# Optimization experiments

Measured on AMD Instinct MI355X. Metric: run time of the kernel, lower is better.

The kernel has to match this reference:

```python
import jax, jax.numpy as jnp
import numpy as np

D_MODEL = 1024
D_STATE = 128
D_CONV = 4
EXPAND = 2
HEADDIM = 64
D_INNER = EXPAND * D_MODEL          # 2048
NHEADS = D_INNER // HEADDIM          # 32
CONV_CH = D_INNER + 2 * D_STATE      # conv acts on x, B, C (ngroups=1)
D_IN_PROJ = 2 * D_INNER + 2 * D_STATE + NHEADS
CHUNK = 128


def setup_inputs() -> dict:
    key = jax.random.key(0)
    ks = jax.random.split(key, 8)
    B, L = 4, 2048
    return {
        'x': jax.random.normal(ks[0], (B, L, D_MODEL), jnp.float32),
        'ln_w': jnp.ones((D_MODEL,), jnp.float32),
        'ln_b': jnp.zeros((D_MODEL,), jnp.float32),
        'in_proj_w': jax.random.normal(ks[1], (D_IN_PROJ, D_MODEL), jnp.float32) * 0.02,
        'conv_w': jax.random.normal(ks[2], (CONV_CH, D_CONV), jnp.float32) * 0.2,
        'conv_b': jnp.zeros((CONV_CH,), jnp.float32),
        'dt_bias': jax.random.normal(ks[3], (NHEADS,), jnp.float32) * 0.5,
        'A_log': jax.random.uniform(ks[4], (NHEADS,), jnp.float32, 0.0, 1.5),
        'D': jax.random.normal(ks[5], (NHEADS,), jnp.float32) * 0.1 + 1.0,
        'norm_w': jnp.ones((D_INNER,), jnp.float32),
        'out_proj_w': jax.random.normal(ks[6], (D_MODEL, D_INNER), jnp.float32) * 0.02,
    }


def segsum(a):
    # a: (..., T) -> (..., T, T) with out[i, j] = sum_{j < k <= i} a[k], -inf above diag
    T = a.shape[-1]
    a_rep = jnp.broadcast_to(a[..., :, None], a.shape + (T,))
    a_masked = jnp.where(jnp.tril(jnp.ones((T, T), bool), -1), a_rep, 0.0)
    seg = jnp.cumsum(a_masked, axis=-2)
    return jnp.where(jnp.tril(jnp.ones((T, T), bool), 0), seg, -jnp.inf)


def _ssd(X, a, Bm, Cm):
    # Chunked SSD (Mamba2). X: (b,l,h,p) pre-multiplied by dt; a: (b,l,h)=dt*A; Bm,Cm: (b,l,n)
    b, l, h, p = X.shape
    c = l // CHUNK
    Xc = X.reshape(b, c, CHUNK, h, p)
    Bc = Bm.reshape(b, c, CHUNK, -1)
    Cc = Cm.reshape(b, c, CHUNK, -1)
    ac = a.reshape(b, c, CHUNK, h).transpose(0, 3, 1, 2)   # (b,h,c,q)
    a_cs = jnp.cumsum(ac, axis=-1)                          # (b,h,c,q)
    Lm = jnp.exp(segsum(ac))                                # (b,h,c,q,q)
    # intra-chunk (diagonal) part
    Y_diag = jnp.einsum('bcln,bcsn,bhcls,bcshp->bclhp', Cc, Bc, Lm, Xc)
    # chunk final states
    decay_states = jnp.exp(a_cs[..., -1:] - a_cs)           # (b,h,c,q)
    states = jnp.einsum('bcln,bhcl,bclhp->bchpn', Bc, decay_states, Xc)
    states = jnp.concatenate([jnp.zeros_like(states[:, :1]), states], axis=1)  # (b,c+1,h,p,n)
    a_chunk = jnp.pad(a_cs[..., -1], ((0, 0), (0, 0), (1, 0)))  # (b,h,c+1)
    decay_chunk = jnp.exp(segsum(a_chunk))                  # (b,h,c+1,c+1)
    prev_states = jnp.einsum('bhzc,bchpn->bzhpn', decay_chunk, states)[:, :-1]  # (b,c,h,p,n)
    # inter-chunk (off-diagonal) part
    Y_off = jnp.einsum('bcln,bchpn,bhcl->bclhp', Cc, prev_states, jnp.exp(a_cs))
    return (Y_diag + Y_off).reshape(b, l, h, p)


def reference(x, ln_w, ln_b, in_proj_w, conv_w, conv_b, dt_bias, A_log, D, norm_w, out_proj_w):
    B, L, _ = x.shape
    # pre-LayerNorm
    mu = x.mean(-1, keepdims=True)
    var = ((x - mu) ** 2).mean(-1, keepdims=True)
    h = (x - mu) / jnp.sqrt(var + 1e-5) * ln_w + ln_b
    # Mamba2 in_proj -> [z, xBC, dt]
    zxbcdt = h @ in_proj_w.T
    z = zxbcdt[..., :D_INNER]
    xBC = zxbcdt[..., D_INNER:D_INNER + CONV_CH]
    dt = jax.nn.softplus(zxbcdt[..., -NHEADS:] + dt_bias)  # (B,L,H)
    # causal depthwise conv1d + SiLU
    xp = jnp.pad(xBC, ((0, 0), (D_CONV - 1, 0), (0, 0)))
    conv = sum(xp[:, k:k + L, :] * conv_w[:, k] for k in range(D_CONV)) + conv_b
    xBC = jax.nn.silu(conv)
    xs = xBC[..., :D_INNER].reshape(B, L, NHEADS, HEADDIM)
    Bm = xBC[..., D_INNER:D_INNER + D_STATE]
    Cm = xBC[..., D_INNER + D_STATE:]
    A = -jnp.exp(A_log)                                    # (H,)
    Y = _ssd(xs * dt[..., None], dt * A, Bm, Cm)
    Y = Y + D[None, None, :, None] * xs                    # D skip connection
    y = Y.reshape(B, L, D_INNER)
    # gated RMSNorm (norm_before_gate=False)
    y = y * jax.nn.silu(z)
    y = y * jax.lax.rsqrt(jnp.mean(y * y, -1, keepdims=True) + 1e-5) * norm_w
    out = y @ out_proj_w.T
    # dropout in eval mode = identity; residual
    return out + x
```

## Files before the change

### kernel.cpp

```cpp
#include <hip/hip_runtime.h>
#include <math.h>

#define BATCH   4
#define LSEQ    2048
#define DMODEL  1024
#define DSTATE  128
#define HEADDIM 64
#define DINNER  2048
#define NHEADS  32
#define CONVCH  2304
#define DINPROJ 4384
#define NPAD    4480
#define CHUNKL  128
#define NCHUNK  16
#define ROWS    (BATCH*LSEQ)

#define B_Z     ((size_t)0)
#define B_XBC   (B_Z   + (size_t)ROWS*DINNER*2)
#define B_DT    (B_XBC + (size_t)ROWS*CONVCH*2)
#define B_XS    (B_DT  + (size_t)ROWS*NHEADS*4)
#define B_BC    (B_XS  + (size_t)ROWS*DINNER*2)
#define B_Y     (B_BC  + (size_t)ROWS*256*2)
#define B_ASUM  (B_Y   + (size_t)ROWS*DINNER*2)
#define B_END   (B_ASUM + (size_t)BATCH*NCHUNK*NHEADS*4)

typedef __attribute__((ext_vector_type(8))) short bf16x8;
typedef __attribute__((ext_vector_type(4))) float f32x4;

__device__ __forceinline__ float b2f(ushort u) {
  union { uint32_t i; float f; } v; v.i = ((uint32_t)u) << 16; return v.f;
}
__device__ __forceinline__ ushort f2b(float f) {
  union { float f; uint32_t i; } v; v.f = f;
  uint32_t r = (v.i + 0x7FFFu + ((v.i >> 16) & 1u)) >> 16;
  return (ushort)r;
}

__device__ __forceinline__ void async_ld16(const void* g, void* l) {
  __builtin_amdgcn_global_load_lds(
      (const __attribute__((address_space(1))) unsigned int*)g,
      (__attribute__((address_space(3))) unsigned int*)l, 16, 0, 0);
}

__global__ __launch_bounds__(256) void convert_win_kernel(const float* __restrict__ W,
                                                          ushort* __restrict__ Wb)
{
  size_t i = (size_t)blockIdx.x*256 + threadIdx.x;
  Wb[i] = (i < (size_t)DINPROJ*DMODEL) ? f2b(W[i]) : (ushort)0;
}

__global__ __launch_bounds__(256) void convert_wout_kernel(const float* __restrict__ W,
                                                           ushort* __restrict__ Wb)
{
  size_t i = (size_t)blockIdx.x*256 + threadIdx.x;
  Wb[i] = f2b(W[i]);
}

__global__ __launch_bounds__(256) void ln_kernel(const float* __restrict__ x,
    const float* __restrict__ w, const float* __restrict__ bias, ushort* __restrict__ h)
{
  const int row = blockIdx.x;
  const int t = threadIdx.x;
  const float* xr = x + (size_t)row * DMODEL;
  float v[4];
  float s = 0.f;
  #pragma unroll
  for (int i = 0; i < 4; i++) { v[i] = xr[t + i*256]; s += v[i]; }
  __shared__ float red[4];
  #pragma unroll
  for (int o = 32; o > 0; o >>= 1) s += __shfl_down(s, o, 64);
  if ((t & 63) == 0) red[t >> 6] = s;
  __syncthreads();
  float mean = (red[0]+red[1]+red[2]+red[3]) * (1.f/DMODEL);
  float vs = 0.f;
  #pragma unroll
  for (int i = 0; i < 4; i++) { float d = v[i]-mean; vs += d*d; }
  #pragma unroll
  for (int o = 32; o > 0; o >>= 1) vs += __shfl_down(vs, o, 64);
  __syncthreads();
  if ((t & 63) == 0) red[t >> 6] = vs;
  __syncthreads();
  float rstd = rsqrtf((red[0]+red[1]+red[2]+red[3]) * (1.f/DMODEL) + 1e-5f);
  ushort* hr = h + (size_t)row * DMODEL;
  #pragma unroll
  for (int i = 0; i < 4; i++) {
    int c = t + i*256;
    hr[c] = f2b((v[i]-mean)*rstd*w[c] + bias[c]);
  }
}

__global__ __launch_bounds__(256) void gemm_inproj_mfma(const ushort* __restrict__ A,
    const ushort* __restrict__ W, ushort* __restrict__ z, ushort* __restrict__ xbc,
    float* __restrict__ dtr)
{
  constexpr int K = DMODEL;
  __shared__ ushort smem[128*136];
  ushort* lA = smem;
  ushort* lB = smem + 4096;
  const int tid = threadIdx.x;
  const int lane = tid & 63;
  const int w = tid >> 6;
  const int m0 = blockIdx.x * 128;
  const int n0 = blockIdx.y * 128;
  const int wm = (w & 1) * 64;
  const int wn = (w >> 1) * 64;
  f32x4 acc[4][4];
  #pragma unroll
  for (int i = 0; i < 4; i++)
    #pragma unroll
    for (int j = 0; j < 4; j++) acc[i][j] = (f32x4)(0.f);

  for (int k0 = 0; k0 < K; k0 += 32) {
    __syncthreads();
    #pragma unroll
    for (int is = 0; is < 2; is++) {
      int c = w*128 + is*64 + lane;
      int row = c >> 2, cb = c & 3;
      async_ld16(A + (size_t)(m0 + row)*K + k0 + cb*8, lA + (size_t)(w*128 + is*64)*8);
      async_ld16(W + (size_t)(n0 + row)*K + k0 + cb*8, lB + (size_t)(w*128 + is*64)*8);
    }
    __syncthreads();
    bf16x8 af[4], bfr[4];
    #pragma unroll
    for (int i = 0; i < 4; i++)
      af[i] = *(const bf16x8*)&lA[(wm + i*16 + (lane & 15))*32 + (lane >> 4)*8];
    #pragma unroll
    for (int j = 0; j < 4; j++)
      bfr[j] = *(const bf16x8*)&lB[(wn + j*16 + (lane & 15))*32 + (lane >> 4)*8];
    #pragma unroll
    for (int i = 0; i < 4; i++)
      #pragma unroll
      for (int j = 0; j < 4; j++)
        acc[i][j] = __builtin_amdgcn_mfma_f32_16x16x32_bf16(af[i], bfr[j], acc[i][j], 0, 0, 0);
  }

  const int col_l = lane & 15;
  const int row_l = (lane >> 4) * 4;
  __syncthreads();
  if (n0 < DINNER + CONVCH) {
    #pragma unroll
    for (int i = 0; i < 4; i++)
      #pragma unroll
      for (int j = 0; j < 4; j++)
        #pragma unroll
        for (int r = 0; r < 4; r++)
          smem[(wm + i*16 + row_l + r)*136 + wn + j*16 + col_l] = f2b(acc[i][j][r]);
    __syncthreads();
    ushort* outp; int coff, ncols;
    if (n0 < DINNER) { outp = z;   coff = n0;          ncols = DINNER; }
    else             { outp = xbc; coff = n0 - DINNER; ncols = CONVCH; }
    #pragma unroll
    for (int it = 0; it < 8; it++) {
      int idx = tid + it*256;
      int row = idx >> 4, c8 = idx & 15;
      *(uint4*)(outp + (size_t)(m0 + row)*ncols + coff + c8*8) = *(const uint4*)&smem[row*136 + c8*8];
    }
  } else {
    #pragma unroll
    for (int i = 0; i < 4; i++)
      #pragma unroll
      for (int j = 0; j < 2; j++) {
        int lc = wn + j*16 + col_l;
        if (lc < 32) {
          #pragma unroll
          for (int r = 0; r < 4; r++)
            dtr[(size_t)(m0 + wm + i*16 + row_l + r)*NHEADS + lc] = acc[i][j][r];
        }
      }
  }
}

__global__ __launch_bounds__(256) void gemm_outproj_mfma(const ushort* __restrict__ A,
    const ushort* __restrict__ W, const float* __restrict__ x, float* __restrict__ out)
{
  constexpr int K = DINNER;
  __shared__ ushort lA[128*32];
  __shared__ ushort lB[128*32];
  const int tid = threadIdx.x;
  const int lane = tid & 63;
  const int w = tid >> 6;
  const int m0 = blockIdx.x * 128;
  const int n0 = blockIdx.y * 128;
  const int wm = (w & 1) * 64;
  const int wn = (w >> 1) * 64;
  f32x4 acc[4][4];
  #pragma unroll
  for (int i = 0; i < 4; i++)
    #pragma unroll
    for (int j = 0; j < 4; j++) acc[i][j] = (f32x4)(0.f);

  for (int k0 = 0; k0 < K; k0 += 32) {
    __syncthreads();
    #pragma unroll
    for (int is = 0; is < 2; is++) {
      int c = w*128 + is*64 + lane;
      int row = c >> 2, cb = c & 3;
      async_ld16(A + (size_t)(m0 + row)*K + k0 + cb*8, lA + (size_t)(w*128 + is*64)*8);
      async_ld16(W + (size_t)(n0 + row)*K + k0 + cb*8, lB + (size_t)(w*128 + is*64)*8);
    }
    __syncthreads();
    bf16x8 af[4], bfr[4];
    #pragma unroll
    for (int i = 0; i < 4; i++)
      af[i] = *(const bf16x8*)&lA[(wm + i*16 + (lane & 15))*32 + (lane >> 4)*8];
    #pragma unroll
    for (int j = 0; j < 4; j++)
      bfr[j] = *(const bf16x8*)&lB[(wn + j*16 + (lane & 15))*32 + (lane >> 4)*8];
    #pragma unroll
    for (int i = 0; i < 4; i++)
      #pragma unroll
      for (int j = 0; j < 4; j++)
        acc[i][j] = __builtin_amdgcn_mfma_f32_16x16x32_bf16(af[i], bfr[j], acc[i][j], 0, 0, 0);
  }

  const int col_l = lane & 15;
  const int row_l = (lane >> 4) * 4;
  #pragma unroll
  for (int i = 0; i < 4; i++) {
    #pragma unroll
    for (int j = 0; j < 4; j++) {
      int gn = n0 + wn + j*16 + col_l;
      #pragma unroll
      for (int r = 0; r < 4; r++) {
        int gm = m0 + wm + i*16 + row_l + r;
        out[(size_t)gm*DMODEL + gn] = acc[i][j][r] + x[(size_t)gm*DMODEL + gn];
      }
    }
  }
}

__global__ __launch_bounds__(256) void dt_kernel(float* __restrict__ dtr, const float* __restrict__ dtb)
{
  int i = blockIdx.x*256 + threadIdx.x;
  float v = dtr[i] + dtb[i & (NHEADS-1)];
  dtr[i] = (v > 20.f) ? v : log1pf(expf(v));
}

__global__ __launch_bounds__(256) void conv_tiled(const ushort* __restrict__ xbc,
    const float* __restrict__ cw, const float* __restrict__ cb,
    ushort* __restrict__ xs, ushort* __restrict__ bcb)
{
  __shared__ ushort tile[35*256];
  const int tid = threadIdx.x;
  const int ch0 = blockIdx.x * 256;
  const int row0 = blockIdx.y * 32;
  const int l0 = row0 & (LSEQ-1);
  for (int idx = tid; idx < 35*32; idx += 256) {
    int r = idx >> 5, c16 = idx & 31;
    uint4 v = make_uint4(0,0,0,0);
    if (l0 + r - 3 >= 0)
      v = *(const uint4*)(xbc + (size_t)(row0 + r - 3)*CONVCH + ch0 + c16*8);
    *(uint4*)&tile[r*256 + c16*8] = v;
  }
  __syncthreads();
  const int ch = ch0 + tid;
  const float w0 = cw[ch*4+0], w1 = cw[ch*4+1], w2 = cw[ch*4+2], w3 = cw[ch*4+3];
  const float bias = cb[ch];
  const bool isX = (ch0 < DINNER);
  #pragma unroll 4
  for (int r = 0; r < 32; r++) {
    float acc = bias;
    acc = fmaf(b2f(tile[(r+0)*256 + tid]), w0, acc);
    acc = fmaf(b2f(tile[(r+1)*256 + tid]), w1, acc);
    acc = fmaf(b2f(tile[(r+2)*256 + tid]), w2, acc);
    acc = fmaf(b2f(tile[(r+3)*256 + tid]), w3, acc);
    float v = acc / (1.f + expf(-acc));
    if (isX) xs[(size_t)(row0 + r)*DINNER + ch] = f2b(v);
    else     bcb[(size_t)(row0 + r)*256 + (ch - DINNER)] = f2b(v);
  }
}

__global__ __launch_bounds__(256) void states_mfma(
    const ushort* __restrict__ xs, const ushort* __restrict__ bcb, const float* __restrict__ dt,
    const float* __restrict__ A_log, ushort* __restrict__ S, float* __restrict__ asum)
{
  constexpr int LDP = 136;
  __shared__ ushort lBT[128*LDP];
  __shared__ ushort lXT[64*LDP];
  __shared__ float dts[CHUNKL], acs[CHUNKL];
  __shared__ float wtot;
  const int hh = blockIdx.x, c = blockIdx.y, b = blockIdx.z;
  const int tid = threadIdx.x;
  const int lane = tid & 63;
  const int w = tid >> 6;
  const int rbase = b*LSEQ + c*CHUNKL;
  const size_t sbase = (size_t)((b*NCHUNK + c)*NHEADS + hh) * 8192;

  float pre = 0.f;
  if (tid < 128) {
    float myv = dt[(size_t)(rbase + tid)*NHEADS + hh];
    dts[tid] = myv;
    pre = myv;
    #pragma unroll
    for (int o = 1; o < 64; o <<= 1) {
      float u = __shfl_up(pre, o, 64);
      if ((tid & 63) >= o) pre += u;
    }
    if (tid == 63) wtot = pre;
  }
  #pragma unroll
  for (int it = 0; it < 8; it++) {
    int chunk = tid + it*256;
    int l = chunk >> 4, n8 = chunk & 15;
    ushort tmp[8];
    *(uint4*)tmp = *(const uint4*)(bcb + (size_t)(rbase + l)*256 + n8*8);
    #pragma unroll
    for (int u = 0; u < 8; u++) lBT[(n8*8+u)*LDP + l] = tmp[u];
  }
  __syncthreads();
  float alast_loc = 0.f;
  if (tid < 128) {
    float Aval = -expf(A_log[hh]);
    float a = (pre + ((tid >= 64) ? wtot : 0.f)) * Aval;
    acs[tid] = a;
    if (tid == 127) { asum[(b*NCHUNK + c)*NHEADS + hh] = a; }
  }
  __syncthreads();
  alast_loc = acs[CHUNKL-1];
  #pragma unroll
  for (int it = 0; it < 4; it++) {
    int chunk = tid + it*256;
    int l = chunk >> 3, p8 = (chunk & 7)*8;
    ushort tmp[8];
    *(uint4*)tmp = *(const uint4*)(xs + (size_t)(rbase + l)*DINNER + hh*HEADDIM + p8);
    float wl = dts[l] * expf(alast_loc - acs[l]);
    #pragma unroll
    for (int u = 0; u < 8; u++) lXT[(p8+u)*LDP + l] = f2b(b2f(tmp[u]) * wl);
  }
  __syncthreads();

  const int rl = lane & 15;
  const int kq = (lane >> 4) * 8;
  const int nb = w * 32;
  f32x4 acc[4][2];
  #pragma unroll
  for (int i = 0; i < 4; i++) { acc[i][0] = (f32x4)(0.f); acc[i][1] = (f32x4)(0.f); }
  #pragma unroll
  for (int k0 = 0; k0 < 128; k0 += 32) {
    bf16x8 af[4], bfr[2];
    #pragma unroll
    for (int i = 0; i < 4; i++) af[i]  = *(const bf16x8*)&lXT[(i*16 + rl)*LDP + k0 + kq];
    #pragma unroll
    for (int j = 0; j < 2; j++) bfr[j] = *(const bf16x8*)&lBT[(nb + j*16 + rl)*LDP + k0 + kq];
    #pragma unroll
    for (int i = 0; i < 4; i++)
      #pragma unroll
      for (int j = 0; j < 2; j++)
        acc[i][j] = __builtin_amdgcn_mfma_f32_16x16x32_bf16(af[i], bfr[j], acc[i][j], 0, 0, 0);
  }
  __syncthreads();
  const int colL = lane & 15;
  const int rowQ = (lane >> 4) * 4;
  #pragma unroll
  for (int i = 0; i < 4; i++)
    #pragma unroll
    for (int j = 0; j < 2; j++)
      #pragma unroll
      for (int r = 0; r < 4; r++)
        lXT[(i*16 + rowQ + r)*LDP + nb + j*16 + colL] = f2b(acc[i][j][r]);
  __syncthreads();
  #pragma unroll
  for (int it = 0; it < 4; it++) {
    int idx = tid + it*256;
    int row = idx >> 4, c8 = idx & 15;
    *(uint4*)(S + sbase + row*128 + c8*8) = *(const uint4*)&lXT[row*LDP + c8*8];
  }
}

__global__ __launch_bounds__(256) void scan_kernel(ushort* __restrict__ S, const float* __restrict__ asum)
{
  const int hh = blockIdx.x, b = blockIdx.y;
  const int tid = threadIdx.x;
  float carry[32];
  #pragma unroll
  for (int i = 0; i < 32; i++) carry[i] = 0.f;
  for (int c = 0; c < NCHUNK; c++) {
    ushort* Sp = S + (size_t)((b*NCHUNK + c)*NHEADS + hh) * 8192;
    float dec = expf(asum[(b*NCHUNK + c)*NHEADS + hh]);
    #pragma unroll
    for (int i = 0; i < 32; i++) {
      float sv = b2f(Sp[tid + i*256]);
      Sp[tid + i*256] = f2b(carry[i]);
      carry[i] = fmaf(dec, carry[i], sv);
    }
  }
}

__global__ __launch_bounds__(256) void yssd_mfma(
    const ushort* __restrict__ xs, const ushort* __restrict__ bcb, const float* __restrict__ dt,
    const float* __restrict__ A_log, const float* __restrict__ Dvec,
    const ushort* __restrict__ S, ushort* __restrict__ y)
{
  constexpr int LDP = 136;
  __shared__ ushort lC [128*LDP];
  __shared__ ushort lBM[128*LDP];
  __shared__ ushort lP [64*LDP];
  __shared__ ushort lXT[64*LDP];
  __shared__ float dts[CHUNKL], acs[CHUNKL];
  __shared__ float wtot;
  const int hh = blockIdx.x, c = blockIdx.y, b = blockIdx.z;
  const int tid = threadIdx.x;
  const int lane = tid & 63;
  const int w = tid >> 6;
  const int rbase = b*LSEQ + c*CHUNKL;
  const size_t sbase = (size_t)((b*NCHUNK + c)*NHEADS + hh) * 8192;

  #pragma unroll
  for (int it = 0; it < 8; it++) {
    int chunk = tid + it*256;
    int l = chunk >> 4, c8 = chunk & 15;
    const ushort* src = bcb + (size_t)(rbase + l)*256 + c8*8;
    *(uint4*)&lBM[l*LDP + c8*8] = *(const uint4*)src;
    *(uint4*)&lC [l*LDP + c8*8] = *(const uint4*)(src + 128);
  }
  #pragma unroll
  for (int it = 0; it < 4; it++) {
    int chunk = tid + it*256;
    int p = chunk >> 4, c8 = chunk & 15;
    *(uint4*)&lP[p*LDP + c8*8] = *(const uint4*)(S + sbase + p*128 + c8*8);
  }
  #pragma unroll
  for (int it = 0; it < 4; it++) {
    int chunk = tid + it*256;
    int s = chunk >> 3, p0 = (chunk & 7)*8;
    ushort tmp[8];
    *(uint4*)tmp = *(const uint4*)(xs + (size_t)(rbase + s)*DINNER + hh*HEADDIM + p0);
    #pragma unroll
    for (int u = 0; u < 8; u++) lXT[(p0+u)*LDP + s] = tmp[u];
  }
  float pre = 0.f;
  if (tid < 128) {
    float myv = dt[(size_t)(rbase + tid)*NHEADS + hh];
    dts[tid] = myv;
    pre = myv;
    #pragma unroll
    for (int o = 1; o < 64; o <<= 1) {
      float u = __shfl_up(pre, o, 64);
      if ((tid & 63) >= o) pre += u;
    }
    if (tid == 63) wtot = pre;
  }
  __syncthreads();
  if (tid < 128) {
    float Aval = -expf(A_log[hh]);
    acs[tid] = (pre + ((tid >= 64) ? wtot : 0.f)) * Aval;
  }

  const int rl = lane & 15;
  const int kq = (lane >> 4) * 8;
  const int colL = lane & 15;
  const int rowQ = (lane >> 4) * 4;

  const int wm = (w & 1) * 64;
  const int wn = (w >> 1) * 64;
  f32x4 G[4][4];
  #pragma unroll
  for (int i = 0; i < 4; i++)
    #pragma unroll
    for (int j = 0; j < 4; j++) G[i][j] = (f32x4)(0.f);
  #pragma unroll
  for (int k0 = 0; k0 < 128; k0 += 32) {
    bf16x8 af[4], bfr[4];
    #pragma unroll
    for (int i = 0; i < 4; i++) af[i]  = *(const bf16x8*)&lC [(wm + i*16 + rl)*LDP + k0 + kq];
    #pragma unroll
    for (int j = 0; j < 4; j++) bfr[j] = *(const bf16x8*)&lBM[(wn + j*16 + rl)*LDP + k0 + kq];
    #pragma unroll
    for (int i = 0; i < 4; i++)
      #pragma unroll
      for (int j = 0; j < 4; j++)
        G[i][j] = __builtin_amdgcn_mfma_f32_16x16x32_bf16(af[i], bfr[j], G[i][j], 0, 0, 0);
  }
  __syncthreads();

  #pragma unroll
  for (int j = 0; j < 4; j++) {
    int sIdx = wn + j*16 + colL;
    float as = acs[sIdx];
    float ds = dts[sIdx];
    #pragma unroll
    for (int i = 0; i < 4; i++) {
      #pragma unroll
      for (int r = 0; r < 4; r++) {
        int lIdx = wm + i*16 + rowQ + r;
        float m = (lIdx >= sIdx) ? G[i][j][r] * expf(acs[lIdx] - as) * ds : 0.f;
        lBM[lIdx*LDP + sIdx] = f2b(m);
      }
    }
  }

  const int om = w * 32;
  f32x4 Y[2][4];
  #pragma unroll
  for (int i = 0; i < 2; i++)
    #pragma unroll
    for (int j = 0; j < 4; j++) Y[i][j] = (f32x4)(0.f);
  #pragma unroll
  for (int k0 = 0; k0 < 128; k0 += 32) {
    bf16x8 a2[2], b2[4];
    #pragma unroll
    for (int i = 0; i < 2; i++) a2[i] = *(const bf16x8*)&lC[(om + i*16 + rl)*LDP + k0 + kq];
    #pragma unroll
    for (int j = 0; j < 4; j++) b2[j] = *(const bf16x8*)&lP[(j*16 + rl)*LDP + k0 + kq];
    #pragma unroll
    for (int i = 0; i < 2; i++)
      #pragma unroll
      for (int j = 0; j < 4; j++)
        Y[i][j] = __builtin_amdgcn_mfma_f32_16x16x32_bf16(a2[i], b2[j], Y[i][j], 0, 0, 0);
  }
  #pragma unroll
  for (int i = 0; i < 2; i++)
    #pragma unroll
    for (int r = 0; r < 4; r++) {
      float e = expf(acs[om + i*16 + rowQ + r]);
      #pragma unroll
      for (int j = 0; j < 4; j++) Y[i][j][r] *= e;
    }
  __syncthreads();

  #pragma unroll
  for (int k0 = 0; k0 < 128; k0 += 32) {
    bf16x8 a3[2], b3[4];
    #pragma unroll
    for (int i = 0; i < 2; i++) a3[i] = *(const bf16x8*)&lBM[(om + i*16 + rl)*LDP + k0 + kq];
    #pragma unroll
    for (int j = 0; j < 4; j++) b3[j] = *(const bf16x8*)&lXT[(j*16 + rl)*LDP + k0 + kq];
    #pragma unroll
    for (int i = 0; i < 2; i++)
      #pragma unroll
      for (int j = 0; j < 4; j++)
        Y[i][j] = __builtin_amdgcn_mfma_f32_16x16x32_bf16(a3[i], b3[j], Y[i][j], 0, 0, 0);
  }

  const float Dh = Dvec[hh];
  #pragma unroll
  for (int i = 0; i < 2; i++) {
    #pragma unroll
    for (int r = 0; r < 4; r++) {
      int lIdx = om + i*16 + rowQ + r;
      ushort* yrow = y + (size_t)(rbase + lIdx)*DINNER + hh*HEADDIM;
      #pragma unroll
      for (int j = 0; j < 4; j++) {
        int p = j*16 + colL;
        float val = Y[i][j][r] + Dh * b2f(lXT[p*LDP + lIdx]);
        yrow[p] = f2b(val);
      }
    }
  }
}

__global__ __launch_bounds__(256) void rmsnorm_kernel(ushort* __restrict__ y,
    const ushort* __restrict__ z, const float* __restrict__ nw)
{
  const int row = blockIdx.x;
  const int t = threadIdx.x;
  ushort* yr = y + (size_t)row*DINNER;
  const ushort* zr = z + (size_t)row*DINNER;
  float v[8];
  float ss = 0.f;
  #pragma unroll
  for (int i = 0; i < 8; i++) {
    int c = t + i*256;
    float zz = b2f(zr[c]);
    float g = b2f(yr[c]) * (zz / (1.f + expf(-zz)));
    v[i] = g;
    ss += g*g;
  }
  #pragma unroll
  for (int o = 32; o > 0; o >>= 1) ss += __shfl_down(ss, o, 64);
  __shared__ float red[4];
  if ((t & 63) == 0) red[t >> 6] = ss;
  __syncthreads();
  float scale = rsqrtf((red[0]+red[1]+red[2]+red[3]) * (1.f/DINNER) + 1e-5f);
  #pragma unroll
  for (int i = 0; i < 8; i++) {
    int c = t + i*256;
    yr[c] = f2b(v[i]*scale*nw[c]);
  }
}

extern "C" void kernel_launch(void* const* d_in, const int* in_sizes, int n_in,
                              void* d_out, int out_size, void* d_ws, size_t ws_size,
                              hipStream_t stream)
{
  const float* x    = (const float*)d_in[0];
  const float* lnw  = (const float*)d_in[1];
  const float* lnb  = (const float*)d_in[2];
  const float* win  = (const float*)d_in[3];
  const float* cw   = (const float*)d_in[4];
  const float* cb   = (const float*)d_in[5];
  const float* dtb  = (const float*)d_in[6];
  const float* alog = (const float*)d_in[7];
  const float* dvec = (const float*)d_in[8];
  const float* nw   = (const float*)d_in[9];
  const float* wout = (const float*)d_in[10];
  float* out = (float*)d_out;
  char* ws = (char*)d_ws;
  (void)in_sizes; (void)n_in; (void)out_size;

  if (ws_size < B_END) return;

  ushort* zb   = (ushort*)(ws + B_Z);
  ushort* xbcb = (ushort*)(ws + B_XBC);
  float*  dtr  = (float*) (ws + B_DT);
  ushort* xsb  = (ushort*)(ws + B_XS);
  ushort* bcb  = (ushort*)(ws + B_BC);
  ushort* yb   = (ushort*)(ws + B_Y);
  float*  asum = (float*) (ws + B_ASUM);
  ushort* Sb   = xbcb;
  ushort* hb   = yb;
  ushort* winB = (ushort*)(ws + B_Y + (size_t)ROWS*DMODEL*2);
  ushort* woutB= (ushort*)(ws + B_XBC + (size_t)BATCH*NCHUNK*NHEADS*HEADDIM*DSTATE*2);

  hipLaunchKernelGGL(convert_win_kernel, dim3((NPAD*DMODEL)/256), dim3(256), 0, stream, win, winB);
  hipLaunchKernelGGL(ln_kernel, dim3(ROWS), dim3(256), 0, stream, x, lnw, lnb, hb);
  hipLaunchKernelGGL(gemm_inproj_mfma, dim3(64, 35), dim3(256), 0, stream, hb, winB, zb, xbcb, dtr);
  hipLaunchKernelGGL(dt_kernel, dim3(ROWS*NHEADS/256), dim3(256), 0, stream, dtr, dtb);
  hipLaunchKernelGGL(conv_tiled, dim3(9, ROWS/32), dim3(256), 0, stream, xbcb, cw, cb, xsb, bcb);
  hipLaunchKernelGGL(convert_wout_kernel, dim3((DMODEL*DINNER)/256), dim3(256), 0, stream, wout, woutB);
  hipLaunchKernelGGL(states_mfma, dim3(NHEADS, NCHUNK, BATCH), dim3(256), 0, stream,
                     xsb, bcb, dtr, alog, Sb, asum);
  hipLaunchKernelGGL(scan_kernel, dim3(NHEADS, BATCH), dim3(256), 0, stream, Sb, asum);
  hipLaunchKernelGGL(yssd_mfma, dim3(NHEADS, NCHUNK, BATCH), dim3(256), 0, stream,
                     xsb, bcb, dtr, alog, dvec, Sb, yb);
  hipLaunchKernelGGL(rmsnorm_kernel, dim3(ROWS), dim3(256), 0, stream, yb, zb, nw);
  hipLaunchKernelGGL(gemm_outproj_mfma, dim3(64, 8), dim3(256), 0, stream, yb, woutB, x, out);
}
```

Baseline: 504.2 us.

## Swizzle GEMM LDS tiles with BK=64, fuse dt softplus, split scan across slices

Both projection GEMMs now share a core that loads 64-wide K tiles into LDS with an XOR swizzle. This halves the number of barrier pairs and cuts LDS bank conflicts on the fragment reads. The dt bias and softplus are folded into the in_proj epilogue, which removes a separate kernel launch. The out_proj epilogue stages results through LDS so the residual add and store use coalesced float4 accesses. The chunk-state scan is split into four slices per head, giving 4x more blocks so more of the GPU is used.

Result: faster. 480.5 us (-4.7%).

```diff
diff --git a/kernel.cpp b/kernel.cpp
--- a/kernel.cpp
+++ b/kernel.cpp
@@ -42,6 +42,50 @@
       (__attribute__((address_space(3))) unsigned int*)l, 16, 0, 0);
 }
 
+template<int K>
+__device__ __forceinline__ void gemm_core_swz(const ushort* __restrict__ A,
+    const ushort* __restrict__ W, int m0, int n0, int tid,
+    ushort* lA, ushort* lB, f32x4 acc[4][4])
+{
+  const int lane = tid & 63;
+  const int w = tid >> 6;
+  const int wm = (w & 1) * 64;
+  const int wn = (w >> 1) * 64;
+  const int rl = lane & 15;
+  const int q  = lane >> 4;
+  for (int k0 = 0; k0 < K; k0 += 64) {
+    __syncthreads();
+    #pragma unroll
+    for (int is = 0; is < 4; is++) {
+      int s = (w*4 + is)*64 + lane;
+      int row = s >> 3;
+      int g = (s & 7) ^ (row & 7);
+      async_ld16(A + (size_t)(m0 + row)*K + k0 + g*8, lA + (size_t)s*8);
+      async_ld16(W + (size_t)(n0 + row)*K + k0 + g*8, lB + (size_t)s*8);
+    }
+    __syncthreads();
+    #pragma unroll
+    for (int kh = 0; kh < 2; kh++) {
+      bf16x8 af[4], bfr[4];
+      #pragma unroll
+      for (int i = 0; i < 4; i++) {
+        int row = wm + i*16 + rl;
+        af[i] = *(const bf16x8*)&lA[(size_t)(row*8 + ((kh*4 + q) ^ (row & 7)))*8];
+      }
+      #pragma unroll
+      for (int j = 0; j < 4; j++) {
+        int row = wn + j*16 + rl;
+        bfr[j] = *(const bf16x8*)&lB[(size_t)(row*8 + ((kh*4 + q) ^ (row & 7)))*8];
+      }
+      #pragma unroll
+      for (int i = 0; i < 4; i++)
+        #pragma unroll
+        for (int j = 0; j < 4; j++)
+          acc[i][j] = __builtin_amdgcn_mfma_f32_16x16x32_bf16(af[i], bfr[j], acc[i][j], 0, 0, 0);
+    }
+  }
+}
+
 __global__ __launch_bounds__(256) void convert_win_kernel(const float* __restrict__ W,
                                                           ushort* __restrict__ Wb)
 {
@@ -91,12 +135,11 @@
 
 __global__ __launch_bounds__(256) void gemm_inproj_mfma(const ushort* __restrict__ A,
     const ushort* __restrict__ W, ushort* __restrict__ z, ushort* __restrict__ xbc,
-    float* __restrict__ dtr)
-{
-  constexpr int K = DMODEL;
+    float* __restrict__ dtr, const float* __restrict__ dtb)
+{
   __shared__ ushort smem[128*136];
   ushort* lA = smem;
-  ushort* lB = smem + 4096;
+  ushort* lB = smem + 8192;
   const int tid = threadIdx.x;
   const int lane = tid & 63;
   const int w = tid >> 6;
@@ -110,29 +153,7 @@
     #pragma unroll
     for (int j = 0; j < 4; j++) acc[i][j] = (f32x4)(0.f);
 
-  for (int k0 = 0; k0 < K; k0 += 32) {
-    __syncthreads();
-    #pragma unroll
-    for (int is = 0; is < 2; is++) {
-      int c = w*128 + is*64 + lane;
-      int row = c >> 2, cb = c & 3;
-      async_ld16(A + (size_t)(m0 + row)*K + k0 + cb*8, lA + (size_t)(w*128 + is*64)*8);
-      async_ld16(W + (size_t)(n0 + row)*K + k0 + cb*8, lB + (size_t)(w*128 + is*64)*8);
-    }
-    __syncthreads();
-    bf16x8 af[4], bfr[4];
-    #pragma unroll
-    for (int i = 0; i < 4; i++)
-      af[i] = *(const bf16x8*)&lA[(wm + i*16 + (lane & 15))*32 + (lane >> 4)*8];
-    #pragma unroll
-    for (int j = 0; j < 4; j++)
-      bfr[j] = *(const bf16x8*)&lB[(wn + j*16 + (lane & 15))*32 + (lane >> 4)*8];
-    #pragma unroll
-    for (int i = 0; i < 4; i++)
-      #pragma unroll
-      for (int j = 0; j < 4; j++)
-        acc[i][j] = __builtin_amdgcn_mfma_f32_16x16x32_bf16(af[i], bfr[j], acc[i][j], 0, 0, 0);
-  }
+  gemm_core_swz<DMODEL>(A, W, m0, n0, tid, lA, lB, acc);
 
   const int col_l = lane & 15;
   const int row_l = (lane >> 4) * 4;
@@ -162,9 +183,13 @@
       for (int j = 0; j < 2; j++) {
         int lc = wn + j*16 + col_l;
         if (lc < 32) {
+          float bb = dtb[lc];
           #pragma unroll
-          for (int r = 0; r < 4; r++)
-            dtr[(size_t)(m0 + wm + i*16 + row_l + r)*NHEADS + lc] = acc[i][j][r];
+          for (int r = 0; r < 4; r++) {
+            float v = acc[i][j][r] + bb;
+            v = (v > 20.f) ? v : log1pf(expf(v));
+            dtr[(size_t)(m0 + wm + i*16 + row_l + r)*NHEADS + lc] = v;
+          }
         }
       }
   }
@@ -173,15 +198,15 @@
 __global__ __launch_bounds__(256) void gemm_outproj_mfma(const ushort* __restrict__ A,
     const ushort* __restrict__ W, const float* __restrict__ x, float* __restrict__ out)
 {
-  constexpr int K = DINNER;
-  __shared__ ushort lA[128*32];
-  __shared__ ushort lB[128*32];
+  __shared__ ushort smem[17408];
+  ushort* lA = smem;
+  ushort* lB = smem + 8192;
+  float* fbuf = (float*)smem;
   const int tid = threadIdx.x;
   const int lane = tid & 63;
   const int w = tid >> 6;
   const int m0 = blockIdx.x * 128;
   const int n0 = blockIdx.y * 128;
-  const int wm = (w & 1) * 64;
   const int wn = (w >> 1) * 64;
   f32x4 acc[4][4];
   #pragma unroll
@@ -189,51 +214,34 @@
     #pragma unroll
     for (int j = 0; j < 4; j++) acc[i][j] = (f32x4)(0.f);
 
-  for (int k0 = 0; k0 < K; k0 += 32) {
+  gemm_core_swz<DINNER>(A, W, m0, n0, tid, lA, lB, acc);
+
+  const int colL = lane & 15;
+  const int rowQ = (lane >> 4) * 4;
+  #pragma unroll
+  for (int h0 = 0; h0 < 2; h0++) {
     __syncthreads();
-    #pragma unroll
-    for (int is = 0; is < 2; is++) {
-      int c = w*128 + is*64 + lane;
-      int row = c >> 2, cb = c & 3;
-      async_ld16(A + (size_t)(m0 + row)*K + k0 + cb*8, lA + (size_t)(w*128 + is*64)*8);
-      async_ld16(W + (size_t)(n0 + row)*K + k0 + cb*8, lB + (size_t)(w*128 + is*64)*8);
+    if ((w & 1) == h0) {
+      #pragma unroll
+      for (int i = 0; i < 4; i++)
+        #pragma unroll
+        for (int j = 0; j < 4; j++)
+          #pragma unroll
+          for (int r = 0; r < 4; r++)
+            fbuf[(i*16 + rowQ + r)*132 + wn + j*16 + colL] = acc[i][j][r];
     }
     __syncthreads();
-    bf16x8 af[4], bfr[4];
-    #pragma unroll
-    for (int i = 0; i < 4; i++)
-      af[i] = *(const bf16x8*)&lA[(wm + i*16 + (lane & 15))*32 + (lane >> 4)*8];
-    #pragma unroll
-    for (int j = 0; j < 4; j++)
-      bfr[j] = *(const bf16x8*)&lB[(wn + j*16 + (lane & 15))*32 + (lane >> 4)*8];
-    #pragma unroll
-    for (int i = 0; i < 4; i++)
-      #pragma unroll
-      for (int j = 0; j < 4; j++)
-        acc[i][j] = __builtin_amdgcn_mfma_f32_16x16x32_bf16(af[i], bfr[j], acc[i][j], 0, 0, 0);
-  }
-
-  const int col_l = lane & 15;
-  const int row_l = (lane >> 4) * 4;
-  #pragma unroll
-  for (int i = 0; i < 4; i++) {
-    #pragma unroll
-    for (int j = 0; j < 4; j++) {
-      int gn = n0 + wn + j*16 + col_l;
-      #pragma unroll
-      for (int r = 0; r < 4; r++) {
-        int gm = m0 + wm + i*16 + row_l + r;
-        out[(size_t)gm*DMODEL + gn] = acc[i][j][r] + x[(size_t)gm*DMODEL + gn];
-      }
-    }
-  }
-}
-
-__global__ __launch_bounds__(256) void dt_kernel(float* __restrict__ dtr, const float* __restrict__ dtb)
-{
-  int i = blockIdx.x*256 + threadIdx.x;
-  float v = dtr[i] + dtb[i & (NHEADS-1)];
-  dtr[i] = (v > 20.f) ? v : log1pf(expf(v));
+    #pragma unroll
+    for (int it = 0; it < 8; it++) {
+      int idx = tid + it*256;
+      int row = idx >> 5, c4 = idx & 31;
+      int gm = m0 + h0*64 + row;
+      float4 xv = *(const float4*)(x + (size_t)gm*DMODEL + n0 + c4*4);
+      float4 vv = *(const float4*)&fbuf[row*132 + c4*4];
+      vv.x += xv.x; vv.y += xv.y; vv.z += xv.z; vv.w += xv.w;
+      *(float4*)(out + (size_t)gm*DMODEL + n0 + c4*4) = vv;
+    }
+  }
 }
 
 __global__ __launch_bounds__(256) void conv_tiled(const ushort* __restrict__ xbc,
@@ -369,18 +377,19 @@
 
 __global__ __launch_bounds__(256) void scan_kernel(ushort* __restrict__ S, const float* __restrict__ asum)
 {
-  const int hh = blockIdx.x, b = blockIdx.y;
-  const int tid = threadIdx.x;
-  float carry[32];
-  #pragma unroll
-  for (int i = 0; i < 32; i++) carry[i] = 0.f;
+  const int hh = blockIdx.x, sl = blockIdx.y, b = blockIdx.z;
+  const int base0 = sl*2048 + threadIdx.x;
+  float carry[8];
+  #pragma unroll
+  for (int i = 0; i < 8; i++) carry[i] = 0.f;
   for (int c = 0; c < NCHUNK; c++) {
     ushort* Sp = S + (size_t)((b*NCHUNK + c)*NHEADS + hh) * 8192;
     float dec = expf(asum[(b*NCHUNK + c)*NHEADS + hh]);
     #pragma unroll
-    for (int i = 0; i < 32; i++) {
-      float sv = b2f(Sp[tid + i*256]);
-      Sp[tid + i*256] = f2b(carry[i]);
+    for (int i = 0; i < 8; i++) {
+      int idx = base0 + i*256;
+      float sv = b2f(Sp[idx]);
+      Sp[idx] = f2b(carry[i]);
       carry[i] = fmaf(dec, carry[i], sv);
     }
   }
@@ -614,13 +623,12 @@
 
   hipLaunchKernelGGL(convert_win_kernel, dim3((NPAD*DMODEL)/256), dim3(256), 0, stream, win, winB);
   hipLaunchKernelGGL(ln_kernel, dim3(ROWS), dim3(256), 0, stream, x, lnw, lnb, hb);
-  hipLaunchKernelGGL(gemm_inproj_mfma, dim3(64, 35), dim3(256), 0, stream, hb, winB, zb, xbcb, dtr);
-  hipLaunchKernelGGL(dt_kernel, dim3(ROWS*NHEADS/256), dim3(256), 0, stream, dtr, dtb);
+  hipLaunchKernelGGL(gemm_inproj_mfma, dim3(64, 35), dim3(256), 0, stream, hb, winB, zb, xbcb, dtr, dtb);
   hipLaunchKernelGGL(conv_tiled, dim3(9, ROWS/32), dim3(256), 0, stream, xbcb, cw, cb, xsb, bcb);
   hipLaunchKernelGGL(convert_wout_kernel, dim3((DMODEL*DINNER)/256), dim3(256), 0, stream, wout, woutB);
   hipLaunchKernelGGL(states_mfma, dim3(NHEADS, NCHUNK, BATCH), dim3(256), 0, stream,
                      xsb, bcb, dtr, alog, Sb, asum);
-  hipLaunchKernelGGL(scan_kernel, dim3(NHEADS, BATCH), dim3(256), 0, stream, Sb, asum);
+  hipLaunchKernelGGL(scan_kernel, dim3(NHEADS, 4, BATCH), dim3(256), 0, stream, Sb, asum);
   hipLaunchKernelGGL(yssd_mfma, dim3(NHEADS, NCHUNK, BATCH), dim3(256), 0, stream,
                      xsb, bcb, dtr, alog, dvec, Sb, yb);
   hipLaunchKernelGGL(rmsnorm_kernel, dim3(ROWS), dim3(256), 0, stream, yb, zb, nw);
```
